# Performance work log

Measured on AMD Instinct MI355X. Metric: run time of the kernel, lower is better.

Reference implementation:

```python
import jax, jax.numpy as jnp
import numpy as np

T = 200000


def _sine_layer(tvec, A, w, phi, phic, wc):
    # tvec: (t,), A/w/phi: (n,1), phic/wc: (1,)
    phi_static = jax.nn.relu(phic)  # (1,)
    w_static = jax.nn.relu(wc)
    ph = jax.nn.relu(phi) + phi_static  # (n,1)
    ww = jax.nn.relu(w) + w_static
    sine = A * jnp.sin(ww * tvec[None, :] + ph)  # (n,t)
    return sine, phi_static, w_static


def _selector_layer(tvec, wave_input, w, phi, phic, wc, phi_prev, w_prev):
    # wave_input: (n,t), w/phi: (m,n), phic/wc/phi_prev/w_prev: (1,)
    # NOTE: phi_prev/w_prev passed but phi_prev flag is False in the network,
    # so they are NOT added (matches torch: `if self.phi_prev and ...`).
    phi_static = jax.nn.relu(phic)
    w_static = jax.nn.relu(wc)
    ph = (jax.nn.relu(phi) + phi_static)[:, :, None]  # (m,n,1)
    ww = (jax.nn.relu(w) + w_static)[:, :, None]
    sine = 0.5 * jnp.sin(ww * tvec[None, None, :] + ph) + 0.5  # (m,n,t)
    out = jnp.einsum('mnt,nt->mt', sine, wave_input)  # (m,t)
    return out, phi_static, w_static


def setup_inputs() -> dict:
    key = jax.random.key(0)
    ks = jax.random.split(key, 18)
    r = lambda k, s: jax.random.normal(k, s, dtype=jnp.float32)
    return {
        'initial_wave_input': r(ks[0], (20, T)),
        'A0': r(ks[1], (20, 1)), 'w0': r(ks[2], (20, 1)), 'phi0': r(ks[3], (20, 1)),
        'wc0': r(ks[4], (1,)), 'phic0': r(ks[5], (1,)),
        'w1': r(ks[6], (25, 20)), 'phi1': r(ks[7], (25, 20)),
        'wc1': r(ks[8], (1,)), 'phic1': r(ks[9], (1,)),
        'w2': r(ks[10], (30, 25)), 'phi2': r(ks[11], (30, 25)),
        'wc2': r(ks[12], (1,)), 'phic2': r(ks[13], (1,)),
        'w3': r(ks[14], (1, 30)), 'phi3': r(ks[15], (1, 30)),
        'wc3': r(ks[16], (1,)), 'phic3': r(ks[17], (1,)),
    }


def reference(initial_wave_input, A0, w0, phi0, wc0, phic0,
              w1, phi1, wc1, phic1, w2, phi2, wc2, phic2,
              w3, phi3, wc3, phic3):
    tvec = jnp.linspace(1.0, 1000.0, T, dtype=jnp.float32)
    # initial_wave_input is an argument of the torch module but is never used.
    s, phi, w = _sine_layer(tvec, A0, w0, phi0, phic0, wc0)
    s, phi, w = _selector_layer(tvec, s, w1, phi1, phic1, wc1, phi, w)
    s, phi, w = _selector_layer(tvec, s, w2, phi2, phic2, wc2, phi, w)
    s, phi, w = _selector_layer(tvec, s, w3, phi3, phic3, wc3, phi, w)
    return s  # (1, t)
```

## Files before the change

### kernel.cpp

```cpp
#include <hip/hip_runtime.h>
#include <hip/hip_bf16.h>

#define T_TOTAL 200000

typedef float v4f __attribute__((ext_vector_type(4)));

__device__ float g_P[4496];

__device__ __forceinline__ float sinp(float rev) {
    float g = __builtin_amdgcn_fractf(rev);
    float h = g - 0.5f;
    float u = h * h;
    float p = fmaf(45.621248f, u, -82.391040f);
    p = fmaf(p, u, 64.671616f);
    p = fmaf(p, u, -19.730960f);
    p = fmaf(p, u, 0.9999618f);
    return p;
}

__global__ void prep_kernel(
    const float* __restrict__ A0,
    const float* __restrict__ w0, const float* __restrict__ phi0,
    const float* __restrict__ wc0, const float* __restrict__ phic0,
    const float* __restrict__ w1, const float* __restrict__ phi1,
    const float* __restrict__ wc1, const float* __restrict__ phic1,
    const float* __restrict__ w2, const float* __restrict__ phi2,
    const float* __restrict__ wc2, const float* __restrict__ phic2,
    const float* __restrict__ w3, const float* __restrict__ phi3,
    const float* __restrict__ wc3, const float* __restrict__ phic3)
{
    const int tid = blockIdx.x * blockDim.x + threadIdx.x;
    const int stride = blockDim.x * gridDim.x;

    const double I2PI = 0.15915494309189535;
    const double D64  = 64.0 * 999.0 / 199999.0;

    const double ws0 = fmax((double)wc0[0], 0.0), ps0 = fmax((double)phic0[0], 0.0);
    const double ws1 = fmax((double)wc1[0], 0.0), ps1 = fmax((double)phic1[0], 0.0);
    const double ws2 = fmax((double)wc2[0], 0.0), ps2 = fmax((double)phic2[0], 0.0);
    const double ws3 = fmax((double)wc3[0], 0.0), ps3 = fmax((double)phic3[0], 0.0);

    for (int n = tid; n < 20; n += stride) {
        double wr = fmax((double)w0[n], 0.0) + ws0;
        g_P[4 * n]     = (float)(wr * I2PI);
        g_P[4 * n + 1] = (float)((fmax((double)phi0[n], 0.0) + ps0) * I2PI + 0.25);
        g_P[4 * n + 2] = (float)(2.0 * cos(wr * D64));
        g_P[4 * n + 3] = A0[n];
    }
    for (int k = tid; k < 20 * 32; k += stride) {
        const int n = k >> 5, m = k & 31;
        float wwf = 0.0f, phf = 0.25f, cf = 2.0f;
        if (m < 25) {
            const int s = m * 20 + n;
            double wr = fmax((double)w1[s], 0.0) + ws1;
            wwf = (float)(wr * I2PI);
            phf = (float)((fmax((double)phi1[s], 0.0) + ps1) * I2PI + 0.25);
            cf  = (float)(2.0 * cos(wr * D64));
        }
        g_P[80 + 96 * n + m]      = wwf;
        g_P[80 + 96 * n + 32 + m] = phf;
        g_P[80 + 96 * n + 64 + m] = cf;
    }
    for (int k = tid; k < 25 * 32; k += stride) {
        const int n = k >> 5, m = k & 31;
        float wwf = 0.0f, phf = 0.25f, cf = 2.0f;
        if (m < 30) {
            const int s = m * 25 + n;
            double wr = fmax((double)w2[s], 0.0) + ws2;
            wwf = (float)(wr * I2PI);
            phf = (float)((fmax((double)phi2[s], 0.0) + ps2) * I2PI + 0.25);
            cf  = (float)(2.0 * cos(wr * D64));
        }
        g_P[2000 + 96 * n + m]      = wwf;
        g_P[2000 + 96 * n + 32 + m] = phf;
        g_P[2000 + 96 * n + 64 + m] = cf;
    }
    for (int k = tid; k < 32; k += stride) {
        float wwf = 0.0f, phf = 0.25f, cf = 2.0f;
        if (k < 30) {
            double wr = fmax((double)w3[k], 0.0) + ws3;
            wwf = (float)(wr * I2PI);
            phf = (float)((fmax((double)phi3[k], 0.0) + ps3) * I2PI + 0.25);
            cf  = (float)(2.0 * cos(wr * D64));
        }
        g_P[4400 + k]      = wwf;
        g_P[4400 + 32 + k] = phf;
        g_P[4400 + 64 + k] = cf;
    }
}

__launch_bounds__(512, 8)
__global__ void wave_main(float* __restrict__ out)
{
    __shared__ float sh1[26 * 256];
    __shared__ float shp[8 * 256];

    const int l = threadIdx.x & 63;
    const int w = __builtin_amdgcn_readfirstlane(threadIdx.x >> 6);
    const int tb = blockIdx.x * 256;
    const float STEP = 999.0f / 199999.0f;

    const float tv0 = fmaf((float)(tb + l), STEP, 1.0f);
    const float tv1 = fmaf((float)(tb + l + 64), STEP, 1.0f);

    float acc1[4][4] = {};
    float sum0[4] = {0.f, 0.f, 0.f, 0.f};
    {
        v4f qN  = *(const v4f*)&g_P[0];
        v4f wwN = *(const v4f*)&g_P[80 + 4 * w];
        v4f phN = *(const v4f*)&g_P[80 + 32 + 4 * w];
        v4f CN  = *(const v4f*)&g_P[80 + 64 + 4 * w];
#pragma clang loop unroll(disable)
        for (int n = 0; n < 20; ++n) {
            const v4f q = qN, ww4 = wwN, ph4 = phN, C4 = CN;
            qN  = *(const v4f*)&g_P[4 * (n + 1)];
            const float* __restrict__ pn = &g_P[80 + 96 * (n + 1) + 4 * w];
            wwN = *(const v4f*)&pn[0];
            phN = *(const v4f*)&pn[32];
            CN  = *(const v4f*)&pn[64];

            float s00 = q[3] * sinp(fmaf(q[0], tv0, q[1]));
            float s01 = q[3] * sinp(fmaf(q[0], tv1, q[1]));
            float s02 = fmaf(q[2], s01, -s00);
            float s03 = fmaf(q[2], s02, -s01);
            sum0[0] += s00; sum0[1] += s01; sum0[2] += s02; sum0[3] += s03;
#pragma unroll
            for (int k = 0; k < 4; ++k) {
                float x0 = sinp(fmaf(ww4[k], tv0, ph4[k]));
                float x1 = sinp(fmaf(ww4[k], tv1, ph4[k]));
                float x2 = fmaf(C4[k], x1, -x0);
                float x3 = fmaf(C4[k], x2, -x1);
                acc1[k][0] = fmaf(x0, s00, acc1[k][0]);
                acc1[k][1] = fmaf(x1, s01, acc1[k][1]);
                acc1[k][2] = fmaf(x2, s02, acc1[k][2]);
                acc1[k][3] = fmaf(x3, s03, acc1[k][3]);
            }
        }
    }
#pragma unroll
    for (int k = 0; k < 4; ++k) {
        if (4 * w + k < 25) {
            v4f v;
#pragma unroll
            for (int j = 0; j < 4; ++j) v[j] = fmaf(0.5f, acc1[k][j], 0.5f * sum0[j]);
            *(v4f*)&sh1[(4 * w + k) * 256 + l * 4] = v;
        }
    }
    __syncthreads();

    float acc2[4][4] = {};
    float sum1[4] = {0.f, 0.f, 0.f, 0.f};
    {
        v4f s1N = *(const v4f*)&sh1[l * 4];
        v4f wwN = *(const v4f*)&g_P[2000 + 4 * w];
        v4f phN = *(const v4f*)&g_P[2000 + 32 + 4 * w];
        v4f CN  = *(const v4f*)&g_P[2000 + 64 + 4 * w];
#pragma clang loop unroll(disable)
        for (int n = 0; n < 25; ++n) {
            const v4f s1 = s1N, ww4 = wwN, ph4 = phN, C4 = CN;
            s1N = *(const v4f*)&sh1[(n + 1) * 256 + l * 4];
            const float* __restrict__ pn = &g_P[2000 + 96 * (n + 1) + 4 * w];
            wwN = *(const v4f*)&pn[0];
            phN = *(const v4f*)&pn[32];
            CN  = *(const v4f*)&pn[64];

            sum1[0] += s1[0]; sum1[1] += s1[1]; sum1[2] += s1[2]; sum1[3] += s1[3];
#pragma unroll
            for (int k = 0; k < 4; ++k) {
                float x0 = sinp(fmaf(ww4[k], tv0, ph4[k]));
                float x1 = sinp(fmaf(ww4[k], tv1, ph4[k]));
                float x2 = fmaf(C4[k], x1, -x0);
                float x3 = fmaf(C4[k], x2, -x1);
                acc2[k][0] = fmaf(x0, s1[0], acc2[k][0]);
                acc2[k][1] = fmaf(x1, s1[1], acc2[k][1]);
                acc2[k][2] = fmaf(x2, s1[2], acc2[k][2]);
                acc2[k][3] = fmaf(x3, s1[3], acc2[k][3]);
            }
        }
    }
    float s2r[4][4];
#pragma unroll
    for (int k = 0; k < 4; ++k)
#pragma unroll
        for (int j = 0; j < 4; ++j)
            s2r[k][j] = fmaf(0.5f, acc2[k][j], 0.5f * sum1[j]);

    float pw[4] = {0.f, 0.f, 0.f, 0.f};
    {
        const float* __restrict__ pb = &g_P[4400 + 4 * w];
#pragma unroll
        for (int k = 0; k < 4; ++k) {
            if (4 * w + k < 30) {
                const float ww = pb[k], ph = pb[32 + k], C = pb[64 + k];
                float x0 = sinp(fmaf(ww, tv0, ph));
                float x1 = sinp(fmaf(ww, tv1, ph));
                float x2 = fmaf(C, x1, -x0);
                float x3 = fmaf(C, x2, -x1);
                pw[0] = fmaf(fmaf(0.5f, x0, 0.5f), s2r[k][0], pw[0]);
                pw[1] = fmaf(fmaf(0.5f, x1, 0.5f), s2r[k][1], pw[1]);
                pw[2] = fmaf(fmaf(0.5f, x2, 0.5f), s2r[k][2], pw[2]);
                pw[3] = fmaf(fmaf(0.5f, x3, 0.5f), s2r[k][3], pw[3]);
            }
        }
    }
#pragma unroll
    for (int j = 0; j < 4; ++j)
        shp[w * 256 + j * 64 + l] = pw[j];
    __syncthreads();

    if (w < 4) {
        float r = 0.0f;
#pragma unroll
        for (int w2 = 0; w2 < 8; ++w2)
            r += shp[w2 * 256 + w * 64 + l];
        const int tt = tb + l + 64 * w;
        if (tt < T_TOTAL) out[tt] = r;
    }
}

extern "C" void kernel_launch(void* const* d_in, const int* in_sizes, int n_in,
                              void* d_out, int out_size, void* d_ws, size_t ws_size,
                              hipStream_t stream) {
    (void)in_sizes; (void)n_in; (void)d_ws; (void)ws_size; (void)out_size;
    const float* A0    = (const float*)d_in[1];
    const float* w0    = (const float*)d_in[2];
    const float* phi0  = (const float*)d_in[3];
    const float* wc0   = (const float*)d_in[4];
    const float* phic0 = (const float*)d_in[5];
    const float* w1    = (const float*)d_in[6];
    const float* phi1  = (const float*)d_in[7];
    const float* wc1   = (const float*)d_in[8];
    const float* phic1 = (const float*)d_in[9];
    const float* w2    = (const float*)d_in[10];
    const float* phi2  = (const float*)d_in[11];
    const float* wc2   = (const float*)d_in[12];
    const float* phic2 = (const float*)d_in[13];
    const float* w3    = (const float*)d_in[14];
    const float* phi3  = (const float*)d_in[15];
    const float* wc3   = (const float*)d_in[16];
    const float* phic3 = (const float*)d_in[17];

    float* out = (float*)d_out;

    hipLaunchKernelGGL(prep_kernel, dim3(6), dim3(256), 0, stream,
                       A0, w0, phi0, wc0, phic0,
                       w1, phi1, wc1, phic1,
                       w2, phi2, wc2, phic2,
                       w3, phi3, wc3, phic3);

    const int grid = (T_TOTAL + 255) / 256;
    hipLaunchKernelGGL(wave_main, dim3(grid), dim3(512), 0, stream, out);
}
```

Measured before the change: 56.27 us.

## Stage parameter table in LDS, relayout shared buffers, unroll inner loops by two

Each block now copies the whole precomputed parameter table from global memory into shared memory at kernel start. All per-iteration parameter loads then read LDS instead of wave-uniform global loads. The sh1 shared buffer switches from an interleaved v4f-per-lane layout to a lane-contiguous scalar layout, and both n-loops are unrolled by two. The launch-bounds occupancy hint drops from 8 to 6 to fit the larger LDS footprint, which adds a copy-plus-barrier prologue per block and may lower occupancy.

New measurement: 56.79 us. Within noise of the previous version (+0.9%).

```diff
diff --git a/kernel.cpp b/kernel.cpp
--- a/kernel.cpp
+++ b/kernel.cpp
@@ -89,11 +89,16 @@
     }
 }
 
-__launch_bounds__(512, 8)
+__launch_bounds__(512, 6)
 __global__ void wave_main(float* __restrict__ out)
 {
-    __shared__ float sh1[26 * 256];
-    __shared__ float shp[8 * 256];
+    __shared__ float S[12944];
+    float* const pp  = S;
+    float* const sh1 = S + 4496;
+    float* const shp = S + 10896;
+
+    for (int i = threadIdx.x; i < 4496; i += 512) pp[i] = g_P[i];
+    __syncthreads();
 
     const int l = threadIdx.x & 63;
     const int w = __builtin_amdgcn_readfirstlane(threadIdx.x >> 6);
@@ -106,15 +111,15 @@
     float acc1[4][4] = {};
     float sum0[4] = {0.f, 0.f, 0.f, 0.f};
     {
-        v4f qN  = *(const v4f*)&g_P[0];
-        v4f wwN = *(const v4f*)&g_P[80 + 4 * w];
-        v4f phN = *(const v4f*)&g_P[80 + 32 + 4 * w];
-        v4f CN  = *(const v4f*)&g_P[80 + 64 + 4 * w];
-#pragma clang loop unroll(disable)
+        v4f qN  = *(const v4f*)&pp[0];
+        v4f wwN = *(const v4f*)&pp[80 + 4 * w];
+        v4f phN = *(const v4f*)&pp[80 + 32 + 4 * w];
+        v4f CN  = *(const v4f*)&pp[80 + 64 + 4 * w];
+#pragma clang loop unroll_count(2)
         for (int n = 0; n < 20; ++n) {
             const v4f q = qN, ww4 = wwN, ph4 = phN, C4 = CN;
-            qN  = *(const v4f*)&g_P[4 * (n + 1)];
-            const float* __restrict__ pn = &g_P[80 + 96 * (n + 1) + 4 * w];
+            qN  = *(const v4f*)&pp[4 * (n + 1)];
+            const float* __restrict__ pn = &pp[80 + 96 * (n + 1) + 4 * w];
             wwN = *(const v4f*)&pn[0];
             phN = *(const v4f*)&pn[32];
             CN  = *(const v4f*)&pn[64];
@@ -140,10 +145,10 @@
 #pragma unroll
     for (int k = 0; k < 4; ++k) {
         if (4 * w + k < 25) {
-            v4f v;
-#pragma unroll
-            for (int j = 0; j < 4; ++j) v[j] = fmaf(0.5f, acc1[k][j], 0.5f * sum0[j]);
-            *(v4f*)&sh1[(4 * w + k) * 256 + l * 4] = v;
+#pragma unroll
+            for (int j = 0; j < 4; ++j)
+                sh1[((4 * w + k) * 4 + j) * 64 + l] =
+                    fmaf(0.5f, acc1[k][j], 0.5f * sum0[j]);
         }
     }
     __syncthreads();
@@ -151,30 +156,37 @@
     float acc2[4][4] = {};
     float sum1[4] = {0.f, 0.f, 0.f, 0.f};
     {
-        v4f s1N = *(const v4f*)&sh1[l * 4];
-        v4f wwN = *(const v4f*)&g_P[2000 + 4 * w];
-        v4f phN = *(const v4f*)&g_P[2000 + 32 + 4 * w];
-        v4f CN  = *(const v4f*)&g_P[2000 + 64 + 4 * w];
-#pragma clang loop unroll(disable)
+        float s1N0 = sh1[(0 * 4 + 0) * 64 + l];
+        float s1N1 = sh1[(0 * 4 + 1) * 64 + l];
+        float s1N2 = sh1[(0 * 4 + 2) * 64 + l];
+        float s1N3 = sh1[(0 * 4 + 3) * 64 + l];
+        v4f wwN = *(const v4f*)&pp[2000 + 4 * w];
+        v4f phN = *(const v4f*)&pp[2000 + 32 + 4 * w];
+        v4f CN  = *(const v4f*)&pp[2000 + 64 + 4 * w];
+#pragma clang loop unroll_count(2)
         for (int n = 0; n < 25; ++n) {
-            const v4f s1 = s1N, ww4 = wwN, ph4 = phN, C4 = CN;
-            s1N = *(const v4f*)&sh1[(n + 1) * 256 + l * 4];
-            const float* __restrict__ pn = &g_P[2000 + 96 * (n + 1) + 4 * w];
+            const float s10 = s1N0, s11 = s1N1, s12 = s1N2, s13 = s1N3;
+            const v4f ww4 = wwN, ph4 = phN, C4 = CN;
+            s1N0 = sh1[((n + 1) * 4 + 0) * 64 + l];
+            s1N1 = sh1[((n + 1) * 4 + 1) * 64 + l];
+            s1N2 = sh1[((n + 1) * 4 + 2) * 64 + l];
+            s1N3 = sh1[((n + 1) * 4 + 3) * 64 + l];
+            const float* __restrict__ pn = &pp[2000 + 96 * (n + 1) + 4 * w];
             wwN = *(const v4f*)&pn[0];
             phN = *(const v4f*)&pn[32];
             CN  = *(const v4f*)&pn[64];
 
-            sum1[0] += s1[0]; sum1[1] += s1[1]; sum1[2] += s1[2]; sum1[3] += s1[3];
+            sum1[0] += s10; sum1[1] += s11; sum1[2] += s12; sum1[3] += s13;
 #pragma unroll
             for (int k = 0; k < 4; ++k) {
                 float x0 = sinp(fmaf(ww4[k], tv0, ph4[k]));
                 float x1 = sinp(fmaf(ww4[k], tv1, ph4[k]));
                 float x2 = fmaf(C4[k], x1, -x0);
                 float x3 = fmaf(C4[k], x2, -x1);
-                acc2[k][0] = fmaf(x0, s1[0], acc2[k][0]);
-                acc2[k][1] = fmaf(x1, s1[1], acc2[k][1]);
-                acc2[k][2] = fmaf(x2, s1[2], acc2[k][2]);
-                acc2[k][3] = fmaf(x3, s1[3], acc2[k][3]);
+                acc2[k][0] = fmaf(x0, s10, acc2[k][0]);
+                acc2[k][1] = fmaf(x1, s11, acc2[k][1]);
+                acc2[k][2] = fmaf(x2, s12, acc2[k][2]);
+                acc2[k][3] = fmaf(x3, s13, acc2[k][3]);
             }
         }
     }
@@ -187,7 +199,7 @@
 
     float pw[4] = {0.f, 0.f, 0.f, 0.f};
     {
-        const float* __restrict__ pb = &g_P[4400 + 4 * w];
+        const float* __restrict__ pb = &pp[4400 + 4 * w];
 #pragma unroll
         for (int k = 0; k < 4; ++k) {
             if (4 * w + k < 30) {
@@ -205,14 +217,14 @@
     }
 #pragma unroll
     for (int j = 0; j < 4; ++j)
-        shp[w * 256 + j * 64 + l] = pw[j];
+        shp[(w * 4 + j) * 64 + l] = pw[j];
     __syncthreads();
 
     if (w < 4) {
         float r = 0.0f;
 #pragma unroll
         for (int w2 = 0; w2 < 8; ++w2)
-            r += shp[w2 * 256 + w * 64 + l];
+            r += shp[(w2 * 4 + w) * 64 + l];
         const int tt = tb + l + 64 * w;
         if (tt < T_TOTAL) out[tt] = r;
     }
```

## Double block size and split selector outputs two per wave with shared layer-0 sines

Applied to the files above, without the earlier changes.

Launches 1024-thread blocks (16 waves) so each wave handles two selector outputs instead of four. Layer-0 sine values are computed once into LDS rather than being recomputed redundantly by every wave. Layers 2 and 3 are fused per wave, so layer-2 results no longer round-trip through LDS. In exchange, LDS use grows, waves 13-15 sit idle in layer 1 and wave 15 in layer 2, the final reduction reads 16 partials instead of 8, and large blocks may limit occupancy.

Result: faster. 52.17 us (-7.3%).

```diff
diff --git a/kernel.cpp b/kernel.cpp
--- a/kernel.cpp
+++ b/kernel.cpp
@@ -89,11 +89,13 @@
     }
 }
 
-__launch_bounds__(512, 8)
+__launch_bounds__(1024, 8)
 __global__ void wave_main(float* __restrict__ out)
 {
-    __shared__ float sh1[26 * 256];
-    __shared__ float shp[8 * 256];
+    __shared__ float S[15616];
+    float* const sh0 = S;
+    float* const sh1 = S + 5120;
+    float* const shp = S + 11520;
 
     const int l = threadIdx.x & 63;
     const int w = __builtin_amdgcn_readfirstlane(threadIdx.x >> 6);
@@ -103,104 +105,131 @@
     const float tv0 = fmaf((float)(tb + l), STEP, 1.0f);
     const float tv1 = fmaf((float)(tb + l + 64), STEP, 1.0f);
 
-    float acc1[4][4] = {};
-    float sum0[4] = {0.f, 0.f, 0.f, 0.f};
     {
-        v4f qN  = *(const v4f*)&g_P[0];
-        v4f wwN = *(const v4f*)&g_P[80 + 4 * w];
-        v4f phN = *(const v4f*)&g_P[80 + 32 + 4 * w];
-        v4f CN  = *(const v4f*)&g_P[80 + 64 + 4 * w];
-#pragma clang loop unroll(disable)
+        v4f q = *(const v4f*)&g_P[4 * w];
+        float x0 = q[3] * sinp(fmaf(q[0], tv0, q[1]));
+        float x1 = q[3] * sinp(fmaf(q[0], tv1, q[1]));
+        float x2 = fmaf(q[2], x1, -x0);
+        float x3 = fmaf(q[2], x2, -x1);
+        sh0[w * 256 +       l] = x0;
+        sh0[w * 256 +  64 + l] = x1;
+        sh0[w * 256 + 128 + l] = x2;
+        sh0[w * 256 + 192 + l] = x3;
+        if (w < 4) {
+            const int n = 16 + w;
+            q = *(const v4f*)&g_P[4 * n];
+            x0 = q[3] * sinp(fmaf(q[0], tv0, q[1]));
+            x1 = q[3] * sinp(fmaf(q[0], tv1, q[1]));
+            x2 = fmaf(q[2], x1, -x0);
+            x3 = fmaf(q[2], x2, -x1);
+            sh0[n * 256 +       l] = x0;
+            sh0[n * 256 +  64 + l] = x1;
+            sh0[n * 256 + 128 + l] = x2;
+            sh0[n * 256 + 192 + l] = x3;
+        }
+    }
+    __syncthreads();
+
+    if (w < 13) {
+        float acc[2][4] = {};
+        float sum0[4] = {0.f, 0.f, 0.f, 0.f};
+        const int m0 = 2 * w;
+#pragma clang loop unroll_count(2)
         for (int n = 0; n < 20; ++n) {
-            const v4f q = qN, ww4 = wwN, ph4 = phN, C4 = CN;
-            qN  = *(const v4f*)&g_P[4 * (n + 1)];
-            const float* __restrict__ pn = &g_P[80 + 96 * (n + 1) + 4 * w];
-            wwN = *(const v4f*)&pn[0];
-            phN = *(const v4f*)&pn[32];
-            CN  = *(const v4f*)&pn[64];
-
-            float s00 = q[3] * sinp(fmaf(q[0], tv0, q[1]));
-            float s01 = q[3] * sinp(fmaf(q[0], tv1, q[1]));
-            float s02 = fmaf(q[2], s01, -s00);
-            float s03 = fmaf(q[2], s02, -s01);
+            const float s00 = sh0[n * 256 +       l];
+            const float s01 = sh0[n * 256 +  64 + l];
+            const float s02 = sh0[n * 256 + 128 + l];
+            const float s03 = sh0[n * 256 + 192 + l];
             sum0[0] += s00; sum0[1] += s01; sum0[2] += s02; sum0[3] += s03;
-#pragma unroll
-            for (int k = 0; k < 4; ++k) {
-                float x0 = sinp(fmaf(ww4[k], tv0, ph4[k]));
-                float x1 = sinp(fmaf(ww4[k], tv1, ph4[k]));
-                float x2 = fmaf(C4[k], x1, -x0);
-                float x3 = fmaf(C4[k], x2, -x1);
-                acc1[k][0] = fmaf(x0, s00, acc1[k][0]);
-                acc1[k][1] = fmaf(x1, s01, acc1[k][1]);
-                acc1[k][2] = fmaf(x2, s02, acc1[k][2]);
-                acc1[k][3] = fmaf(x3, s03, acc1[k][3]);
-            }
-        }
-    }
-#pragma unroll
-    for (int k = 0; k < 4; ++k) {
-        if (4 * w + k < 25) {
-            v4f v;
-#pragma unroll
-            for (int j = 0; j < 4; ++j) v[j] = fmaf(0.5f, acc1[k][j], 0.5f * sum0[j]);
-            *(v4f*)&sh1[(4 * w + k) * 256 + l * 4] = v;
+            const float* __restrict__ pb = &g_P[80 + 96 * n + m0];
+            const float wwa = pb[0],  wwb = pb[1];
+            const float pha = pb[32], phb = pb[33];
+            const float Ca  = pb[64], Cb  = pb[65];
+            {
+                float x0 = sinp(fmaf(wwa, tv0, pha));
+                float x1 = sinp(fmaf(wwa, tv1, pha));
+                float x2 = fmaf(Ca, x1, -x0);
+                float x3 = fmaf(Ca, x2, -x1);
+                acc[0][0] = fmaf(x0, s00, acc[0][0]);
+                acc[0][1] = fmaf(x1, s01, acc[0][1]);
+                acc[0][2] = fmaf(x2, s02, acc[0][2]);
+                acc[0][3] = fmaf(x3, s03, acc[0][3]);
+            }
+            {
+                float x0 = sinp(fmaf(wwb, tv0, phb));
+                float x1 = sinp(fmaf(wwb, tv1, phb));
+                float x2 = fmaf(Cb, x1, -x0);
+                float x3 = fmaf(Cb, x2, -x1);
+                acc[1][0] = fmaf(x0, s00, acc[1][0]);
+                acc[1][1] = fmaf(x1, s01, acc[1][1]);
+                acc[1][2] = fmaf(x2, s02, acc[1][2]);
+                acc[1][3] = fmaf(x3, s03, acc[1][3]);
+            }
+        }
+#pragma unroll
+        for (int j = 0; j < 4; ++j)
+            sh1[m0 * 256 + j * 64 + l] = fmaf(0.5f, acc[0][j], 0.5f * sum0[j]);
+        if (m0 + 1 < 25) {
+#pragma unroll
+            for (int j = 0; j < 4; ++j)
+                sh1[(m0 + 1) * 256 + j * 64 + l] = fmaf(0.5f, acc[1][j], 0.5f * sum0[j]);
         }
     }
     __syncthreads();
 
-    float acc2[4][4] = {};
-    float sum1[4] = {0.f, 0.f, 0.f, 0.f};
-    {
-        v4f s1N = *(const v4f*)&sh1[l * 4];
-        v4f wwN = *(const v4f*)&g_P[2000 + 4 * w];
-        v4f phN = *(const v4f*)&g_P[2000 + 32 + 4 * w];
-        v4f CN  = *(const v4f*)&g_P[2000 + 64 + 4 * w];
-#pragma clang loop unroll(disable)
+    float pw[4] = {0.f, 0.f, 0.f, 0.f};
+    if (w < 15) {
+        float acc[2][4] = {};
+        float sum1[4] = {0.f, 0.f, 0.f, 0.f};
+        const int m0 = 2 * w;
+#pragma clang loop unroll_count(2)
         for (int n = 0; n < 25; ++n) {
-            const v4f s1 = s1N, ww4 = wwN, ph4 = phN, C4 = CN;
-            s1N = *(const v4f*)&sh1[(n + 1) * 256 + l * 4];
-            const float* __restrict__ pn = &g_P[2000 + 96 * (n + 1) + 4 * w];
-            wwN = *(const v4f*)&pn[0];
-            phN = *(const v4f*)&pn[32];
-            CN  = *(const v4f*)&pn[64];
-
-            sum1[0] += s1[0]; sum1[1] += s1[1]; sum1[2] += s1[2]; sum1[3] += s1[3];
-#pragma unroll
-            for (int k = 0; k < 4; ++k) {
-                float x0 = sinp(fmaf(ww4[k], tv0, ph4[k]));
-                float x1 = sinp(fmaf(ww4[k], tv1, ph4[k]));
-                float x2 = fmaf(C4[k], x1, -x0);
-                float x3 = fmaf(C4[k], x2, -x1);
-                acc2[k][0] = fmaf(x0, s1[0], acc2[k][0]);
-                acc2[k][1] = fmaf(x1, s1[1], acc2[k][1]);
-                acc2[k][2] = fmaf(x2, s1[2], acc2[k][2]);
-                acc2[k][3] = fmaf(x3, s1[3], acc2[k][3]);
-            }
-        }
-    }
-    float s2r[4][4];
-#pragma unroll
-    for (int k = 0; k < 4; ++k)
-#pragma unroll
-        for (int j = 0; j < 4; ++j)
-            s2r[k][j] = fmaf(0.5f, acc2[k][j], 0.5f * sum1[j]);
-
-    float pw[4] = {0.f, 0.f, 0.f, 0.f};
-    {
-        const float* __restrict__ pb = &g_P[4400 + 4 * w];
-#pragma unroll
-        for (int k = 0; k < 4; ++k) {
-            if (4 * w + k < 30) {
-                const float ww = pb[k], ph = pb[32 + k], C = pb[64 + k];
-                float x0 = sinp(fmaf(ww, tv0, ph));
-                float x1 = sinp(fmaf(ww, tv1, ph));
-                float x2 = fmaf(C, x1, -x0);
-                float x3 = fmaf(C, x2, -x1);
-                pw[0] = fmaf(fmaf(0.5f, x0, 0.5f), s2r[k][0], pw[0]);
-                pw[1] = fmaf(fmaf(0.5f, x1, 0.5f), s2r[k][1], pw[1]);
-                pw[2] = fmaf(fmaf(0.5f, x2, 0.5f), s2r[k][2], pw[2]);
-                pw[3] = fmaf(fmaf(0.5f, x3, 0.5f), s2r[k][3], pw[3]);
-            }
+            const float s10 = sh1[n * 256 +       l];
+            const float s11 = sh1[n * 256 +  64 + l];
+            const float s12 = sh1[n * 256 + 128 + l];
+            const float s13 = sh1[n * 256 + 192 + l];
+            sum1[0] += s10; sum1[1] += s11; sum1[2] += s12; sum1[3] += s13;
+            const float* __restrict__ pb = &g_P[2000 + 96 * n + m0];
+            const float wwa = pb[0],  wwb = pb[1];
+            const float pha = pb[32], phb = pb[33];
+            const float Ca  = pb[64], Cb  = pb[65];
+            {
+                float x0 = sinp(fmaf(wwa, tv0, pha));
+                float x1 = sinp(fmaf(wwa, tv1, pha));
+                float x2 = fmaf(Ca, x1, -x0);
+                float x3 = fmaf(Ca, x2, -x1);
+                acc[0][0] = fmaf(x0, s10, acc[0][0]);
+                acc[0][1] = fmaf(x1, s11, acc[0][1]);
+                acc[0][2] = fmaf(x2, s12, acc[0][2]);
+                acc[0][3] = fmaf(x3, s13, acc[0][3]);
+            }
+            {
+                float x0 = sinp(fmaf(wwb, tv0, phb));
+                float x1 = sinp(fmaf(wwb, tv1, phb));
+                float x2 = fmaf(Cb, x1, -x0);
+                float x3 = fmaf(Cb, x2, -x1);
+                acc[1][0] = fmaf(x0, s10, acc[1][0]);
+                acc[1][1] = fmaf(x1, s11, acc[1][1]);
+                acc[1][2] = fmaf(x2, s12, acc[1][2]);
+                acc[1][3] = fmaf(x3, s13, acc[1][3]);
+            }
+        }
+        const float* __restrict__ p3 = &g_P[4400 + m0];
+#pragma unroll
+        for (int k = 0; k < 2; ++k) {
+            const float ww = p3[k], ph = p3[32 + k], C = p3[64 + k];
+            float x0 = sinp(fmaf(ww, tv0, ph));
+            float x1 = sinp(fmaf(ww, tv1, ph));
+            float x2 = fmaf(C, x1, -x0);
+            float x3 = fmaf(C, x2, -x1);
+            const float s20 = fmaf(0.5f, acc[k][0], 0.5f * sum1[0]);
+            const float s21 = fmaf(0.5f, acc[k][1], 0.5f * sum1[1]);
+            const float s22 = fmaf(0.5f, acc[k][2], 0.5f * sum1[2]);
+            const float s23 = fmaf(0.5f, acc[k][3], 0.5f * sum1[3]);
+            pw[0] = fmaf(fmaf(0.5f, x0, 0.5f), s20, pw[0]);
+            pw[1] = fmaf(fmaf(0.5f, x1, 0.5f), s21, pw[1]);
+            pw[2] = fmaf(fmaf(0.5f, x2, 0.5f), s22, pw[2]);
+            pw[3] = fmaf(fmaf(0.5f, x3, 0.5f), s23, pw[3]);
         }
     }
 #pragma unroll
@@ -211,9 +240,9 @@
     if (w < 4) {
         float r = 0.0f;
 #pragma unroll
-        for (int w2 = 0; w2 < 8; ++w2)
+        for (int w2 = 0; w2 < 16; ++w2)
             r += shp[w2 * 256 + w * 64 + l];
-        const int tt = tb + l + 64 * w;
+        const int tt = tb + 64 * w + l;
         if (tt < T_TOTAL) out[tt] = r;
     }
 }
@@ -249,5 +278,5 @@
                        w3, phi3, wc3, phic3);
 
     const int grid = (T_TOTAL + 255) / 256;
-    hipLaunchKernelGGL(wave_main, dim3(grid), dim3(512), 0, stream, out);
-}
+    hipLaunchKernelGGL(wave_main, dim3(grid), dim3(1024), 0, stream, out);
+}
```
